# Kernel tuning notes

Measured on AMD Instinct MI355X. Metric: run time of the kernel, lower is better.

Reference implementation:

```python
import jax, jax.numpy as jnp
import numpy as np

B = 32768   # batch (agents)
H = 64      # h_dim
E = 16      # embedding_dim
M = 6       # num_modes (n_samples)
P = M * 2   # traj_points
T = 30      # pred_len (seq_len)


def setup_inputs() -> dict:
    key = jax.random.key(0)
    ks = jax.random.split(key, 14)
    def s(k, shape, scale=0.1):
        return jax.random.normal(k, shape, jnp.float32) * scale
    return dict(
        traj_abs=s(ks[0], (1, B, 2), 1.0),
        traj_rel=s(ks[1], (1, B, 2), 1.0),
        h0=s(ks[2], (1, B, H)),
        c0=s(ks[3], (1, B, H)),
        W_ih=s(ks[4], (4 * H, E)),
        W_hh=s(ks[5], (4 * H, H)),
        b_ih=s(ks[6], (4 * H,)),
        b_hh=s(ks[7], (4 * H,)),
        W_se=s(ks[8], (E, P)),
        b_se=s(ks[9], (E,)),
        W_pos=s(ks[10], (P, H)),
        b_pos=s(ks[11], (P,)),
        W_conf=s(ks[12], (M, H)),
        b_conf=s(ks[13], (M,)),
    )


def reference(traj_abs, traj_rel, h0, c0, W_ih, W_hh, b_ih, b_hh,
              W_se, b_se, W_pos, b_pos, W_conf, b_conf):
    b = traj_rel.shape[1]
    # repeat_interleave the (x,y) pair num_modes times along feature dim -> [b, 12]
    rel12 = jnp.tile(traj_rel.reshape(b, 1, 2), (1, M, 1)).reshape(b, P)
    x = jax.nn.leaky_relu(rel12 @ W_se.T + b_se)  # [b, E]
    h = h0[0]
    c = c0[0]

    def step(carry, _):
        x, h, c = carry
        # PyTorch LSTM cell, gate order i, f, g, o
        gates = x @ W_ih.T + b_ih + h @ W_hh.T + b_hh  # [b, 4H]
        i, f, g, o = jnp.split(gates, 4, axis=-1)
        c = jax.nn.sigmoid(f) * c + jax.nn.sigmoid(i) * jnp.tanh(g)
        h = jax.nn.sigmoid(o) * jnp.tanh(c)
        rel = h @ W_pos.T + b_pos                      # [b, P]
        x = jax.nn.leaky_relu(rel @ W_se.T + b_se)     # [b, E]
        return (x, h, c), rel

    (x, h, c), rels = jax.lax.scan(step, (x, h, c), None, length=T)  # rels: [T, b, P]
    pred = rels.reshape(T, b, M, 2).transpose(1, 2, 0, 3)            # [b, M, T, 2]
    conf = jax.nn.softmax(h @ W_conf.T + b_conf, axis=1)             # [b, M]
    return pred, conf
```

## Files before the change

kernel.cpp:

```cpp
#include <hip/hip_runtime.h>
#include <hip/hip_bf16.h>

typedef _Float16 half8 __attribute__((ext_vector_type(8)));
typedef _Float16 half4 __attribute__((ext_vector_type(4)));
typedef float float4v __attribute__((ext_vector_type(4)));

#define BATCH 32768
#define TT 30

#if __has_builtin(__builtin_amdgcn_exp2f)
#define FEXP2(x) __builtin_amdgcn_exp2f(x)
#else
#define FEXP2(x) __expf((x) * 0.6931471805599453f)
#endif
#if __has_builtin(__builtin_amdgcn_rcpf)
#define FRCP(x) __builtin_amdgcn_rcpf(x)
#else
#define FRCP(x) (1.0f / (x))
#endif

#define NLOG2E  -1.4426950408889634f
#define N2LOG2E -2.8853900817779268f

#define WFRAG_OFF 0
#define WCF_OFF   12288
#define BIASB_OFF 13312
#define SXY_OFF   13568
#define CBIAS_OFF 13616
#define WCONF_OFF 13648
#define BCONF_OFF 14032
#define FLAG_IDX  14038
#define CONF_BASE (BATCH * 360)

__global__ void detect_kernel(const unsigned short* __restrict__ raw,
                              int* __restrict__ flag_out) {
    __shared__ int sflag[256];
    int local = 0;
    for (int i = threadIdx.x; i < 16384; i += 256) {
        unsigned short u = raw[i];
        if ((u & 0x7F80u) == 0x7F80u) local = 1;
    }
    sflag[threadIdx.x] = local;
    __syncthreads();
    if (threadIdx.x == 0) {
        int f = 0;
        for (int i = 0; i < 256; ++i) f |= sflag[i];
        flag_out[0] = f;
    }
}

__device__ __forceinline__ float ldin(const void* p, int i, int isf32) {
    return isf32 ? ((const float*)p)[i]
                 : (float)((const __hip_bfloat16*)p)[i];
}

__global__ void prep_kernel(const void* __restrict__ W_ih,
                            const void* __restrict__ W_hh,
                            const void* __restrict__ b_ih,
                            const void* __restrict__ b_hh,
                            const void* __restrict__ W_se,
                            const void* __restrict__ b_se,
                            const void* __restrict__ W_pos,
                            const void* __restrict__ b_pos,
                            const void* __restrict__ W_conf,
                            const void* __restrict__ b_conf,
                            float* __restrict__ ws)
{
    const int isf32 = ((const int*)(ws + FLAG_IDX))[0];
    int tid = blockIdx.x * blockDim.x + threadIdx.x;
    int stride = gridDim.x * blockDim.x;
    _Float16* wfh = (_Float16*)ws;

    for (int idx = tid; idx < 24576; idx += stride) {
        int jj = idx & 7, r = idx >> 3;
        int lane = r & 63; r >>= 6;
        int ks = r % 3; r /= 3;
        int gate = r & 3; int wv = r >> 2;
        int col = lane & 15, akq = lane >> 4;
        int k = ks * 32 + akq * 8 + jj;
        int row = gate * 64 + wv * 16 + col;
        float v = 0.f;
        if (k < 16) v = ldin(W_ih, row * 16 + k, isf32);
        else if (k < 80) v = ldin(W_hh, row * 64 + (k - 16), isf32);
        else if (k == 80) v = ldin(b_ih, row, isf32) + ldin(b_hh, row, isf32);
        v *= (gate == 2) ? N2LOG2E : NLOG2E;
        wfh[idx] = (_Float16)v;
    }
    _Float16* wch = (_Float16*)(ws + WCF_OFF);
    for (int idx = tid; idx < 2048; idx += stride) {
        int jj = idx & 7, r = idx >> 3;
        int lane = r & 63; r >>= 6;
        int ks = r & 1, role = r >> 1;
        int col = lane & 15, akq = lane >> 4;
        int k = ks * 32 + akq * 8 + jj;
        float v = 0.f;
        if (role == 0) {
            if (col < 12) v = ldin(W_pos, col * 64 + k, isf32);
        } else {
            float s = 0.f;
            for (int p = 0; p < 12; ++p)
                s += ldin(W_se, col * 12 + p, isf32) * ldin(W_pos, p * 64 + k, isf32);
            v = s;
        }
        wch[idx] = (_Float16)v;
    }
    for (int idx = tid; idx < 256; idx += stride) {
        int gate = idx >> 6;
        float scale = (gate == 2) ? N2LOG2E : NLOG2E;
        ws[BIASB_OFF + idx] = (ldin(b_ih, idx, isf32) + ldin(b_hh, idx, isf32)) * scale;
    }
    for (int idx = tid; idx < 16; idx += stride) {
        float sx = 0.f, sy = 0.f;
        for (int m = 0; m < 6; ++m) {
            sx += ldin(W_se, idx * 12 + 2 * m, isf32);
            sy += ldin(W_se, idx * 12 + 2 * m + 1, isf32);
        }
        ws[SXY_OFF + idx * 3 + 0] = sx;
        ws[SXY_OFF + idx * 3 + 1] = sy;
        ws[SXY_OFF + idx * 3 + 2] = ldin(b_se, idx, isf32);
    }
    for (int idx = tid; idx < 32; idx += stride) {
        int w = idx >> 4, cc = idx & 15;
        float v = 0.f;
        if (w == 0) {
            if (cc < 12) v = ldin(b_pos, cc, isf32);
        } else {
            float s = ldin(b_se, cc, isf32);
            for (int p = 0; p < 12; ++p)
                s += ldin(W_se, cc * 12 + p, isf32) * ldin(b_pos, p, isf32);
            v = s;
        }
        ws[CBIAS_OFF + idx] = v;
    }
    for (int idx = tid; idx < 384; idx += stride)
        ws[WCONF_OFF + idx] = ldin(W_conf, idx, isf32);
    for (int idx = tid; idx < 6; idx += stride)
        ws[BCONF_OFF + idx] = ldin(b_conf, idx, isf32);
}

__global__ __launch_bounds__(256, 4) void lstm_kernel(
    const void* __restrict__ traj_rel,
    const void* __restrict__ h0,
    const void* __restrict__ c0,
    const float* __restrict__ ws,
    float* __restrict__ out)
{
    __shared__ _Float16 zsh[2 * 16 * 168];
    __shared__ _Float16 predh[32 * 30 * 12];

    const int tid = threadIdx.x;
    const int lane = tid & 63;
    const int wid = __builtin_amdgcn_readfirstlane(tid >> 6);
    const int role = wid & 1;
    const int col16 = lane & 15;
    const int akq = lane >> 4;
    const int base = blockIdx.x * 32;
    const int isf32 = ((const int*)(ws + FLAG_IDX))[0];

    const float4v* wfg = (const float4v*)ws;
    half8 Bf[4][3];
#pragma unroll
    for (int tl = 0; tl < 4; ++tl)
#pragma unroll
        for (int ks = 0; ks < 3; ++ks)
            Bf[tl][ks] = __builtin_bit_cast(half8,
                wfg[((wid * 4 + tl) * 3 + ks) * 64 + lane]);
    half8 wfc[2];
    {
        const float4v* wcg = (const float4v*)(ws + WCF_OFF);
#pragma unroll
        for (int ks = 0; ks < 2; ++ks)
            wfc[ks] = __builtin_bit_cast(half8, wcg[(role * 2 + ks) * 64 + lane]);
    }
    const float4v cb4 = *(const float4v*)&ws[CBIAS_OFF + role * 16 + akq * 4];

    float cg0[4], cg1[4];
#pragma unroll
    for (int i = 0; i < 4; ++i) {
        int unit = wid * 16 + akq * 4 + i;
        cg0[i] = ldin(c0, (base + col16) * 64 + unit, isf32);
        cg1[i] = ldin(c0, (base + 16 + col16) * 64 + unit, isf32);
    }
    {
        int m = tid & 31, jq2 = tid >> 5;
        int g = m >> 4, row = m & 15;
        _Float16* zr = &zsh[g * 2688 + row * 168];
        half8 ha;
#pragma unroll
        for (int i = 0; i < 8; ++i)
            ha[i] = (_Float16)ldin(h0, (base + m) * 64 + jq2 * 8 + i, isf32);
        *(half8*)&zr[32 + jq2 * 8] = ha;
        if (jq2 < 4) {
            float rx = ldin(traj_rel, 2 * (base + m), isf32);
            float ry = ldin(traj_rel, 2 * (base + m) + 1, isf32);
            half4 xs;
#pragma unroll
            for (int i = 0; i < 4; ++i) {
                int e = 4 * jq2 + i;
                float x = fmaf(rx, ws[SXY_OFF + e * 3],
                          fmaf(ry, ws[SXY_OFF + e * 3 + 1], ws[SXY_OFF + e * 3 + 2]));
                xs[i] = (_Float16)(x > 0.f ? x : 0.01f * x);
            }
            *(half4*)&zr[4 * jq2] = xs;
        } else if (jq2 == 4) {
            half8 zz = {};
            zz[0] = (_Float16)1.0f;
            *(half8*)&zr[16] = zz;
        } else if (jq2 == 5) {
            half8 zz = {};
            *(half8*)&zr[24] = zz;
        }
    }
    __syncthreads();

    int aoff[2][3];
#pragma unroll
    for (int p = 0; p < 2; ++p)
#pragma unroll
        for (int ks = 0; ks < 3; ++ks) {
            int q = ks * 4 + akq;
            int off = (q < 2) ? q * 8
                    : (q < 10) ? 32 + p * 64 + (q - 2) * 8
                               : 16 + (q - 10) * 8;
            aoff[p][ks] = col16 * 168 + off;
        }
    const int zcb = col16 * 168 + 32 + akq * 8;
    const int hw4 = col16 * 168 + 32 + wid * 16 + akq * 4;
    const int xw4 = col16 * 168 + akq * 4;

#define ZG(g) (&zsh[(g) * 2688])

#define PHASE_AB(ZG_, PC, PN, CARR) do {                                      \
    float4v acc_[4];                                                          \
    _Pragma("unroll")                                                         \
    for (int g = 0; g < 4; ++g) {                                             \
        acc_[g][0] = 0.f; acc_[g][1] = 0.f; acc_[g][2] = 0.f; acc_[g][3] = 0.f;\
    }                                                                         \
    _Pragma("unroll")                                                         \
    for (int ks = 0; ks < 3; ++ks) {                                          \
        half8 af_ = *(const half8*)&(ZG_)[aoff[PC][ks]];                      \
        _Pragma("unroll")                                                     \
        for (int g = 0; g < 4; ++g)                                           \
            acc_[g] = __builtin_amdgcn_mfma_f32_16x16x32_f16(                 \
                Bf[g][ks], af_, acc_[g], 0, 0, 0);                            \
    }                                                                         \
    half4 hv_;                                                                \
    _Pragma("unroll")                                                         \
    for (int i = 0; i < 4; ++i) {                                             \
        float ei = FEXP2(acc_[0][i]);                                         \
        float ef = FEXP2(acc_[1][i]);                                         \
        float eg = FEXP2(acc_[2][i]);                                         \
        float eo = FEXP2(acc_[3][i]);                                         \
        float pp = (1.f + ei) * (1.f + eg);                                   \
        float qq = 1.f + ef;                                                  \
        float cn = fmaf((CARR)[i], pp, (1.f - eg) * qq) * FRCP(pp * qq);      \
        (CARR)[i] = cn;                                                       \
        float ec = FEXP2(cn * N2LOG2E);                                       \
        float hn = (1.f - ec) * FRCP((1.f + eo) * (1.f + ec));                \
        hv_[i] = (_Float16)hn;                                                \
    }                                                                         \
    *(half4*)&(ZG_)[hw4 + (PN) * 64] = hv_;                                   \
} while (0)

#define PHASE_C(ZG_, P, T, GI) do {                                           \
    float4v racc_;                                                            \
    racc_[0] = cb4[0]; racc_[1] = cb4[1]; racc_[2] = cb4[2]; racc_[3] = cb4[3];\
    _Pragma("unroll")                                                         \
    for (int ks = 0; ks < 2; ++ks) {                                          \
        half8 af_ = *(const half8*)&(ZG_)[zcb + (P) * 64 + ks * 32];          \
        racc_ = __builtin_amdgcn_mfma_f32_16x16x32_f16(                       \
            wfc[ks], af_, racc_, 0, 0, 0);                                    \
    }                                                                         \
    if (role == 0) {                                                          \
        if (akq < 3) {                                                        \
            half4 pv_;                                                        \
            _Pragma("unroll")                                                 \
            for (int i = 0; i < 4; ++i) pv_[i] = (_Float16)racc_[i];          \
            *(half4*)&predh[(((GI) * 16 + col16) * 30 + (T)) * 12 + akq * 4] = pv_;\
        }                                                                     \
    } else if ((T) != TT - 1) {                                               \
        half4 xv4_;                                                           \
        _Pragma("unroll")                                                     \
        for (int i = 0; i < 4; ++i) {                                         \
            float xv_ = racc_[i];                                             \
            xv4_[i] = (_Float16)(xv_ > 0.f ? xv_ : 0.01f * xv_);              \
        }                                                                     \
        *(half4*)&(ZG_)[xw4] = xv4_;                                          \
    }                                                                         \
} while (0)

    _Float16* const zg0p = ZG(0);
    _Float16* const zg1p = ZG(1);

    PHASE_AB(zg0p, 0, 1, cg0);
    __syncthreads();
    PHASE_AB(zg1p, 0, 1, cg1);
    if (wid < 2) PHASE_C(zg0p, 1, 0, 0);
    __syncthreads();

    for (int t = 1; t < TT - 1; t += 2) {
        PHASE_AB(zg0p, 1, 0, cg0);
        if (wid >= 2) PHASE_C(zg1p, 1, t - 1, 1);
        __syncthreads();
        PHASE_AB(zg1p, 1, 0, cg1);
        if (wid < 2) PHASE_C(zg0p, 0, t, 0);
        __syncthreads();
        PHASE_AB(zg0p, 0, 1, cg0);
        if (wid >= 2) PHASE_C(zg1p, 0, t, 1);
        __syncthreads();
        PHASE_AB(zg1p, 0, 1, cg1);
        if (wid < 2) PHASE_C(zg0p, 1, t + 1, 0);
        __syncthreads();
    }
    PHASE_AB(zg0p, 1, 0, cg0);
    if (wid >= 2) PHASE_C(zg1p, 1, TT - 2, 1);
    __syncthreads();
    PHASE_AB(zg1p, 1, 0, cg1);
    if (wid < 2) PHASE_C(zg0p, 0, TT - 1, 0);
    __syncthreads();
    if (wid >= 2) PHASE_C(zg1p, 0, TT - 1, 1);
    __syncthreads();

    {
        float4* po4 = (float4*)(out + (size_t)base * 360);
#pragma unroll 1
        for (int q2 = 0; q2 < 12; ++q2) {
            int idx4 = q2 * 256 + tid;
            if (idx4 < 2880) {
                int a = idx4 / 90, rem = idx4 % 90;
                int m = rem / 15, tq = rem % 15;
                int t0 = tq * 2;
                float4 o;
                o.x = (float)predh[(a * 30 + t0) * 12 + 2 * m];
                o.y = (float)predh[(a * 30 + t0) * 12 + 2 * m + 1];
                o.z = (float)predh[(a * 30 + t0 + 1) * 12 + 2 * m];
                o.w = (float)predh[(a * 30 + t0 + 1) * 12 + 2 * m + 1];
                po4[idx4] = o;
            }
        }
    }

    if (wid == 0 && lane < 32) {
        int m = lane;
        int g = m >> 4, row = m & 15;
        float l[6];
#pragma unroll
        for (int md = 0; md < 6; ++md) l[md] = ws[BCONF_OFF + md];
        for (int jj = 0; jj < 64; ++jj) {
            float hv = (float)zsh[g * 2688 + row * 168 + 32 + jj];
#pragma unroll
            for (int md = 0; md < 6; ++md)
                l[md] = fmaf(hv, ws[WCONF_OFF + md * 64 + jj], l[md]);
        }
        float mx = l[0];
#pragma unroll
        for (int md = 1; md < 6; ++md) mx = fmaxf(mx, l[md]);
        float ex[6], s = 0.f;
#pragma unroll
        for (int md = 0; md < 6; ++md) { ex[md] = __expf(l[md] - mx); s += ex[md]; }
        float inv = FRCP(s);
#pragma unroll
        for (int md = 0; md < 6; ++md)
            out[CONF_BASE + (size_t)(base + m) * 6 + md] = ex[md] * inv;
    }
}

extern "C" void kernel_launch(void* const* d_in, const int* in_sizes, int n_in,
                              void* d_out, int out_size, void* d_ws, size_t ws_size,
                              hipStream_t stream) {
    const void* traj_rel = d_in[1];
    const void* h0   = d_in[2];
    const void* c0   = d_in[3];
    const void* W_ih = d_in[4];
    const void* W_hh = d_in[5];
    const void* b_ih = d_in[6];
    const void* b_hh = d_in[7];
    const void* W_se = d_in[8];
    const void* b_se = d_in[9];
    const void* W_pos  = d_in[10];
    const void* b_pos  = d_in[11];
    const void* W_conf = d_in[12];
    const void* b_conf = d_in[13];
    float* ws = (float*)d_ws;
    float* out = (float*)d_out;

    detect_kernel<<<1, 256, 0, stream>>>((const unsigned short*)W_hh,
                                         (int*)(ws + FLAG_IDX));
    prep_kernel<<<40, 256, 0, stream>>>(W_ih, W_hh, b_ih, b_hh, W_se, b_se,
                                        W_pos, b_pos, W_conf, b_conf, ws);
    lstm_kernel<<<BATCH / 32, 256, 0, stream>>>(traj_rel, h0, c0, ws, out);
}
```

Before: 197.9 us.

## Halve per-block batch to 16 agents, shrink LDS, stream predictions in chunks

```diff
diff --git a/kernel.cpp b/kernel.cpp
--- a/kernel.cpp
+++ b/kernel.cpp
@@ -3,6 +3,7 @@
 
 typedef _Float16 half8 __attribute__((ext_vector_type(8)));
 typedef _Float16 half4 __attribute__((ext_vector_type(4)));
+typedef _Float16 half2v __attribute__((ext_vector_type(2)));
 typedef float float4v __attribute__((ext_vector_type(4)));
 
 #define BATCH 32768
@@ -138,23 +139,22 @@
         ws[BCONF_OFF + idx] = ldin(b_conf, idx, isf32);
 }
 
-__global__ __launch_bounds__(256, 4) void lstm_kernel(
+__global__ __launch_bounds__(256, 8) void lstm_kernel(
     const void* __restrict__ traj_rel,
     const void* __restrict__ h0,
     const void* __restrict__ c0,
     const float* __restrict__ ws,
     float* __restrict__ out)
 {
-    __shared__ _Float16 zsh[2 * 16 * 168];
-    __shared__ _Float16 predh[32 * 30 * 12];
+    __shared__ __align__(16) _Float16 zsh[16 * 168];
+    __shared__ __align__(16) _Float16 predh[16 * 11 * 12];
 
     const int tid = threadIdx.x;
     const int lane = tid & 63;
     const int wid = __builtin_amdgcn_readfirstlane(tid >> 6);
-    const int role = wid & 1;
     const int col16 = lane & 15;
     const int akq = lane >> 4;
-    const int base = blockIdx.x * 32;
+    const int base = blockIdx.x * 16;
     const int isf32 = ((const int*)(ws + FLAG_IDX))[0];
 
     const float4v* wfg = (const float4v*)ws;
@@ -165,6 +165,7 @@
         for (int ks = 0; ks < 3; ++ks)
             Bf[tl][ks] = __builtin_bit_cast(half8,
                 wfg[((wid * 4 + tl) * 3 + ks) * 64 + lane]);
+    const int role = wid & 1;
     half8 wfc[2];
     {
         const float4v* wcg = (const float4v*)(ws + WCF_OFF);
@@ -174,39 +175,38 @@
     }
     const float4v cb4 = *(const float4v*)&ws[CBIAS_OFF + role * 16 + akq * 4];
 
-    float cg0[4], cg1[4];
-#pragma unroll
-    for (int i = 0; i < 4; ++i) {
-        int unit = wid * 16 + akq * 4 + i;
-        cg0[i] = ldin(c0, (base + col16) * 64 + unit, isf32);
-        cg1[i] = ldin(c0, (base + 16 + col16) * 64 + unit, isf32);
-    }
+    float c[4];
+#pragma unroll
+    for (int i = 0; i < 4; ++i)
+        c[i] = ldin(c0, (base + col16) * 64 + wid * 16 + akq * 4 + i, isf32);
+
     {
-        int m = tid & 31, jq2 = tid >> 5;
-        int g = m >> 4, row = m & 15;
-        _Float16* zr = &zsh[g * 2688 + row * 168];
-        half8 ha;
-#pragma unroll
-        for (int i = 0; i < 8; ++i)
-            ha[i] = (_Float16)ldin(h0, (base + m) * 64 + jq2 * 8 + i, isf32);
-        *(half8*)&zr[32 + jq2 * 8] = ha;
-        if (jq2 < 4) {
+        int m = tid & 15, jq2 = tid >> 4;
+        _Float16* zr = &zsh[m * 168];
+        if (jq2 < 8) {
+            half8 ha;
+#pragma unroll
+            for (int i = 0; i < 8; ++i)
+                ha[i] = (_Float16)ldin(h0, (base + m) * 64 + jq2 * 8 + i, isf32);
+            *(half8*)&zr[32 + jq2 * 8] = ha;
+        } else if (jq2 < 12) {
+            int jx = jq2 - 8;
             float rx = ldin(traj_rel, 2 * (base + m), isf32);
             float ry = ldin(traj_rel, 2 * (base + m) + 1, isf32);
             half4 xs;
 #pragma unroll
             for (int i = 0; i < 4; ++i) {
-                int e = 4 * jq2 + i;
+                int e = 4 * jx + i;
                 float x = fmaf(rx, ws[SXY_OFF + e * 3],
                           fmaf(ry, ws[SXY_OFF + e * 3 + 1], ws[SXY_OFF + e * 3 + 2]));
                 xs[i] = (_Float16)(x > 0.f ? x : 0.01f * x);
             }
-            *(half4*)&zr[4 * jq2] = xs;
-        } else if (jq2 == 4) {
+            *(half4*)&zr[4 * jx] = xs;
+        } else if (jq2 == 12) {
             half8 zz = {};
             zz[0] = (_Float16)1.0f;
             *(half8*)&zr[16] = zz;
-        } else if (jq2 == 5) {
+        } else if (jq2 == 13) {
             half8 zz = {};
             *(half8*)&zr[24] = zz;
         }
@@ -228,9 +228,9 @@
     const int hw4 = col16 * 168 + 32 + wid * 16 + akq * 4;
     const int xw4 = col16 * 168 + akq * 4;
 
-#define ZG(g) (&zsh[(g) * 2688])
-
-#define PHASE_AB(ZG_, PC, PN, CARR) do {                                      \
+#define SLOT(T) ((T) - ((T) >= 22 ? 22 : (T) >= 11 ? 11 : 0))
+
+#define PHASE_AB(PC, PN) do {                                                 \
     float4v acc_[4];                                                          \
     _Pragma("unroll")                                                         \
     for (int g = 0; g < 4; ++g) {                                             \
@@ -238,7 +238,7 @@
     }                                                                         \
     _Pragma("unroll")                                                         \
     for (int ks = 0; ks < 3; ++ks) {                                          \
-        half8 af_ = *(const half8*)&(ZG_)[aoff[PC][ks]];                      \
+        half8 af_ = *(const half8*)&zsh[aoff[PC][ks]];                        \
         _Pragma("unroll")                                                     \
         for (int g = 0; g < 4; ++g)                                           \
             acc_[g] = __builtin_amdgcn_mfma_f32_16x16x32_f16(                 \
@@ -253,115 +253,110 @@
         float eo = FEXP2(acc_[3][i]);                                         \
         float pp = (1.f + ei) * (1.f + eg);                                   \
         float qq = 1.f + ef;                                                  \
-        float cn = fmaf((CARR)[i], pp, (1.f - eg) * qq) * FRCP(pp * qq);      \
-        (CARR)[i] = cn;                                                       \
+        float cn = fmaf(c[i], pp, (1.f - eg) * qq) * FRCP(pp * qq);           \
+        c[i] = cn;                                                            \
         float ec = FEXP2(cn * N2LOG2E);                                       \
         float hn = (1.f - ec) * FRCP((1.f + eo) * (1.f + ec));                \
         hv_[i] = (_Float16)hn;                                                \
     }                                                                         \
-    *(half4*)&(ZG_)[hw4 + (PN) * 64] = hv_;                                   \
+    *(half4*)&zsh[hw4 + (PN) * 64] = hv_;                                     \
 } while (0)
 
-#define PHASE_C(ZG_, P, T, GI) do {                                           \
-    float4v racc_;                                                            \
-    racc_[0] = cb4[0]; racc_[1] = cb4[1]; racc_[2] = cb4[2]; racc_[3] = cb4[3];\
+#define PHASE_C(P, T, LAST) do {                                              \
+    if (wid < 2) {                                                            \
+        float4v racc_;                                                        \
+        racc_[0] = cb4[0]; racc_[1] = cb4[1];                                 \
+        racc_[2] = cb4[2]; racc_[3] = cb4[3];                                 \
+        _Pragma("unroll")                                                     \
+        for (int ks = 0; ks < 2; ++ks) {                                      \
+            half8 af_ = *(const half8*)&zsh[zcb + (P) * 64 + ks * 32];        \
+            racc_ = __builtin_amdgcn_mfma_f32_16x16x32_f16(                   \
+                wfc[ks], af_, racc_, 0, 0, 0);                                \
+        }                                                                     \
+        if (wid == 0) {                                                       \
+            if (akq < 3) {                                                    \
+                int st_ = SLOT(T);                                            \
+                half4 pv_;                                                    \
+                _Pragma("unroll")                                             \
+                for (int i = 0; i < 4; ++i) pv_[i] = (_Float16)racc_[i];      \
+                *(half4*)&predh[(col16 * 11 + st_) * 12 + akq * 4] = pv_;     \
+            }                                                                 \
+        } else if (!(LAST)) {                                                 \
+            half4 xv4_;                                                       \
+            _Pragma("unroll")                                                 \
+            for (int i = 0; i < 4; ++i) {                                     \
+                float xv_ = racc_[i];                                         \
+                xv4_[i] = (_Float16)(xv_ > 0.f ? xv_ : 0.01f * xv_);          \
+            }                                                                 \
+            *(half4*)&zsh[xw4] = xv4_;                                        \
+        }                                                                     \
+    }                                                                         \
+} while (0)
+
+#define FLUSH(T0) do {                                                        \
+    float4* po4_ = (float4*)(out + (size_t)base * 360);                       \
     _Pragma("unroll")                                                         \
-    for (int ks = 0; ks < 2; ++ks) {                                          \
-        half8 af_ = *(const half8*)&(ZG_)[zcb + (P) * 64 + ks * 32];          \
-        racc_ = __builtin_amdgcn_mfma_f32_16x16x32_f16(                       \
-            wfc[ks], af_, racc_, 0, 0, 0);                                    \
-    }                                                                         \
-    if (role == 0) {                                                          \
-        if (akq < 3) {                                                        \
-            half4 pv_;                                                        \
-            _Pragma("unroll")                                                 \
-            for (int i = 0; i < 4; ++i) pv_[i] = (_Float16)racc_[i];          \
-            *(half4*)&predh[(((GI) * 16 + col16) * 30 + (T)) * 12 + akq * 4] = pv_;\
+    for (int q2 = 0; q2 < 2; ++q2) {                                          \
+        int idx4 = q2 * 256 + tid;                                            \
+        if (idx4 < 480) {                                                     \
+            int a = idx4 / 30, rem = idx4 % 30;                               \
+            int m = rem / 5, tq = rem % 5;                                    \
+            int t0 = (T0) + tq * 2;                                           \
+            int s0 = SLOT(t0), s1 = SLOT(t0 + 1);                             \
+            half2v p0 = *(const half2v*)&predh[(a * 11 + s0) * 12 + 2 * m];   \
+            half2v p1 = *(const half2v*)&predh[(a * 11 + s1) * 12 + 2 * m];   \
+            float4 o;                                                         \
+            o.x = (float)p0[0]; o.y = (float)p0[1];                           \
+            o.z = (float)p1[0]; o.w = (float)p1[1];                           \
+            po4_[a * 90 + m * 15 + ((T0) >> 1) + tq] = o;                     \
         }                                                                     \
-    } else if ((T) != TT - 1) {                                               \
-        half4 xv4_;                                                           \
-        _Pragma("unroll")                                                     \
-        for (int i = 0; i < 4; ++i) {                                         \
-            float xv_ = racc_[i];                                             \
-            xv4_[i] = (_Float16)(xv_ > 0.f ? xv_ : 0.01f * xv_);              \
-        }                                                                     \
-        *(half4*)&(ZG_)[xw4] = xv4_;                                          \
     }                                                                         \
 } while (0)
 
-    _Float16* const zg0p = ZG(0);
-    _Float16* const zg1p = ZG(1);
-
-    PHASE_AB(zg0p, 0, 1, cg0);
-    __syncthreads();
-    PHASE_AB(zg1p, 0, 1, cg1);
-    if (wid < 2) PHASE_C(zg0p, 1, 0, 0);
-    __syncthreads();
-
-    for (int t = 1; t < TT - 1; t += 2) {
-        PHASE_AB(zg0p, 1, 0, cg0);
-        if (wid >= 2) PHASE_C(zg1p, 1, t - 1, 1);
+    for (int t = 0; t < TT; t += 2) {
+        if (t == 10) FLUSH(0);
+        else if (t == 20) FLUSH(10);
+        PHASE_AB(0, 1);
         __syncthreads();
-        PHASE_AB(zg1p, 1, 0, cg1);
-        if (wid < 2) PHASE_C(zg0p, 0, t, 0);
+        PHASE_C(1, t, 0);
         __syncthreads();
-        PHASE_AB(zg0p, 0, 1, cg0);
-        if (wid >= 2) PHASE_C(zg1p, 0, t, 1);
+        PHASE_AB(1, 0);
         __syncthreads();
-        PHASE_AB(zg1p, 0, 1, cg1);
-        if (wid < 2) PHASE_C(zg0p, 1, t + 1, 0);
+        PHASE_C(0, t + 1, (t + 1) == TT - 1);
         __syncthreads();
     }
-    PHASE_AB(zg0p, 1, 0, cg0);
-    if (wid >= 2) PHASE_C(zg1p, 1, TT - 2, 1);
-    __syncthreads();
-    PHASE_AB(zg1p, 1, 0, cg1);
-    if (wid < 2) PHASE_C(zg0p, 0, TT - 1, 0);
-    __syncthreads();
-    if (wid >= 2) PHASE_C(zg1p, 0, TT - 1, 1);
-    __syncthreads();
-
-    {
-        float4* po4 = (float4*)(out + (size_t)base * 360);
-#pragma unroll 1
-        for (int q2 = 0; q2 < 12; ++q2) {
-            int idx4 = q2 * 256 + tid;
-            if (idx4 < 2880) {
-                int a = idx4 / 90, rem = idx4 % 90;
-                int m = rem / 15, tq = rem % 15;
-                int t0 = tq * 2;
-                float4 o;
-                o.x = (float)predh[(a * 30 + t0) * 12 + 2 * m];
-                o.y = (float)predh[(a * 30 + t0) * 12 + 2 * m + 1];
-                o.z = (float)predh[(a * 30 + t0 + 1) * 12 + 2 * m];
-                o.w = (float)predh[(a * 30 + t0 + 1) * 12 + 2 * m + 1];
-                po4[idx4] = o;
-            }
-        }
-    }
-
-    if (wid == 0 && lane < 32) {
-        int m = lane;
-        int g = m >> 4, row = m & 15;
+    FLUSH(20);
+
+    if (wid == 0) {
+        int r = lane >> 2, qq = lane & 3;
         float l[6];
 #pragma unroll
-        for (int md = 0; md < 6; ++md) l[md] = ws[BCONF_OFF + md];
-        for (int jj = 0; jj < 64; ++jj) {
-            float hv = (float)zsh[g * 2688 + row * 168 + 32 + jj];
+        for (int md = 0; md < 6; ++md)
+            l[md] = (qq == 0) ? ws[BCONF_OFF + md] : 0.f;
+#pragma unroll
+        for (int jj = 0; jj < 16; ++jj) {
+            float hv = (float)zsh[r * 168 + 32 + qq * 16 + jj];
 #pragma unroll
             for (int md = 0; md < 6; ++md)
-                l[md] = fmaf(hv, ws[WCONF_OFF + md * 64 + jj], l[md]);
-        }
-        float mx = l[0];
-#pragma unroll
-        for (int md = 1; md < 6; ++md) mx = fmaxf(mx, l[md]);
-        float ex[6], s = 0.f;
-#pragma unroll
-        for (int md = 0; md < 6; ++md) { ex[md] = __expf(l[md] - mx); s += ex[md]; }
-        float inv = FRCP(s);
-#pragma unroll
-        for (int md = 0; md < 6; ++md)
-            out[CONF_BASE + (size_t)(base + m) * 6 + md] = ex[md] * inv;
+                l[md] = fmaf(hv, ws[WCONF_OFF + md * 64 + qq * 16 + jj], l[md]);
+        }
+#pragma unroll
+        for (int md = 0; md < 6; ++md) {
+            l[md] += __shfl_xor(l[md], 1);
+            l[md] += __shfl_xor(l[md], 2);
+        }
+        if (qq == 0) {
+            float mx = l[0];
+#pragma unroll
+            for (int md = 1; md < 6; ++md) mx = fmaxf(mx, l[md]);
+            float ex[6], s = 0.f;
+#pragma unroll
+            for (int md = 0; md < 6; ++md) { ex[md] = __expf(l[md] - mx); s += ex[md]; }
+            float inv = FRCP(s);
+#pragma unroll
+            for (int md = 0; md < 6; ++md)
+                out[CONF_BASE + (size_t)(base + r) * 6 + md] = ex[md] * inv;
+        }
     }
 }
 
@@ -388,5 +383,5 @@
                                          (int*)(ws + FLAG_IDX));
     prep_kernel<<<40, 256, 0, stream>>>(W_ih, W_hh, b_ih, b_hh, W_se, b_se,
                                         W_pos, b_pos, W_conf, b_conf, ws);
-    lstm_kernel<<<BATCH / 32, 256, 0, stream>>>(traj_rel, h0, c0, ws, out);
-}
+    lstm_kernel<<<BATCH / 16, 256, 0, stream>>>(traj_rel, h0, c0, ws, out);
+}
```

Result: slower. 448.6 us (+126.7%).
